# Kernel optimization log

Measured on AMD Instinct MI355X. Metric: run time of the kernel, lower is better.

Reference implementation:

```python
import math
import jax, jax.numpy as jnp
import numpy as np

T = 2048       # sequence_length
H = 2048       # hidden_size
NH = 32        # num_attention_heads
NKV = 8        # num_key_value_heads
HD = 64        # head_dim
SW = 128       # sliding_window
QM = NH // NKV # q_mult (GQA group size)
ROPE_THETA = 10000.0
EPS = 1e-5


def setup_inputs() -> dict:
    key = jax.random.key(0)
    k_x, k_s, k_qkv, k_out = jax.random.split(key, 4)
    x = jax.random.normal(k_x, (T, H), dtype=jnp.float32)
    scale = jnp.ones((H,), dtype=jnp.float32)
    sinks = jax.random.normal(k_s, (NH,), dtype=jnp.float32) * 0.02
    qkv_dim = HD * (NH + 2 * NKV)  # 3072
    qkv_kernel = jax.random.normal(k_qkv, (H, qkv_dim), dtype=jnp.float32) * (1.0 / math.sqrt(H))
    qkv_bias = jnp.zeros((qkv_dim,), dtype=jnp.float32)
    out_kernel = jax.random.normal(k_out, (H, H), dtype=jnp.float32) * (1.0 / math.sqrt(H))
    out_bias = jnp.zeros((H,), dtype=jnp.float32)
    # RoPE tables: [T, HD//2]
    half = HD // 2
    inv_freq = 1.0 / (ROPE_THETA ** (np.arange(half, dtype=np.float64) / half))
    ang = np.outer(np.arange(T, dtype=np.float64), inv_freq)
    cos_table = jnp.asarray(np.cos(ang), dtype=jnp.float32)
    sin_table = jnp.asarray(np.sin(ang), dtype=jnp.float32)
    # causal + sliding-window additive mask [T, T]
    qp = np.arange(T, dtype=np.int32)[:, None]
    kp = np.arange(T, dtype=np.int32)[None, :]
    m = np.where(kp > qp, -np.inf, 0.0) + np.where(qp - kp > SW, -np.inf, 0.0)
    mask = jnp.asarray(m, dtype=jnp.float32)
    return dict(x=x, scale=scale, sinks=sinks, qkv_kernel=qkv_kernel,
                qkv_bias=qkv_bias, out_kernel=out_kernel, out_bias=out_bias,
                cos_table=cos_table, sin_table=sin_table, mask=mask)


def _rmsnorm(x, scale):
    t = x.astype(jnp.float32)
    rms = jnp.sqrt(jnp.mean(t * t, axis=-1, keepdims=True) + EPS)
    return ((t / rms) * scale).astype(x.dtype)


def _rope(x, cos, sin):
    # x: [T, ..., HD]; split-half rotation as in the reference RotaryEmbedding
    shp = x.shape
    xr = x.reshape(shp[0], -1, HD)
    c = cos[:, None, :].astype(xr.dtype)
    s = sin[:, None, :].astype(xr.dtype)
    x1, x2 = jnp.split(xr, 2, axis=-1)
    y = jnp.concatenate([x1 * c - x2 * s, x2 * c + x1 * s], axis=-1)
    return y.reshape(shp)


def reference(x, scale, sinks, qkv_kernel, qkv_bias, out_kernel, out_bias,
              cos_table, sin_table, mask):
    normed = _rmsnorm(x, scale)
    qkv = normed @ qkv_kernel + qkv_bias                 # [T, 3072]
    q_end = NH * HD
    k_end = q_end + NKV * HD
    q = qkv[:, :q_end].reshape(T, NKV, QM, HD)           # [T, nkv, qm, hd]
    k = qkv[:, q_end:k_end].reshape(T, NKV, HD)          # [T, nkv, hd]
    v = qkv[:, k_end:].reshape(T, NKV, HD)               # [T, nkv, hd]
    q = _rope(q, cos_table, sin_table)
    k = _rope(k, cos_table, sin_table)
    sm_scale = 1.0 / math.sqrt(float(HD))
    # GQA attention without materializing repeated K/V
    logits = jnp.einsum('qnmd,knd->nmqk', q, k) * sm_scale  # [nkv, qm, T, T]
    logits = logits + mask[None, None, :, :]
    sink_col = jnp.broadcast_to(sinks.reshape(NKV, QM, 1, 1), (NKV, QM, T, 1))
    logits = jnp.concatenate([logits, sink_col], axis=-1)   # [nkv, qm, T, T+1]
    weights = jax.nn.softmax(logits, axis=-1)[..., :-1]     # drop sink column
    attn = jnp.einsum('nmqk,knd->qnmd', weights, v).reshape(T, NH * HD)
    projected = attn @ out_kernel + out_bias
    return x + projected
```

## Files before the change

### kernel.cpp

```cpp
#include <hip/hip_runtime.h>
#include <hip/hip_bf16.h>
#include <stdint.h>

typedef __bf16 bf16_t;
typedef __attribute__((ext_vector_type(8))) __bf16 bf16x8;
typedef __attribute__((ext_vector_type(4))) __bf16 bf16x4;
typedef __attribute__((ext_vector_type(4))) float f32x4;

static constexpr int T_SEQ = 2048;
static constexpr int HID   = 2048;
static constexpr int NHEAD = 32;
static constexpr int NKVH  = 8;
static constexpr int HDIM  = 64;
static constexpr int QKVD  = 3072;

__device__ inline f32x4 mfma16(bf16x8 a, bf16x8 b, f32x4 c) {
    return __builtin_amdgcn_mfma_f32_16x16x32_bf16(a, b, c, 0, 0, 0);
}

__device__ inline void load_lds16(const bf16_t* g, bf16_t* l) {
    __builtin_amdgcn_global_load_lds(
        (const __attribute__((address_space(1))) void*)g,
        (__attribute__((address_space(3))) void*)l, 16, 0, 0);
}

__global__ __launch_bounds__(256) void prep_kernel(const float* __restrict__ Wq,
                                                   const float* __restrict__ Wo,
                                                   bf16_t* __restrict__ Tq,
                                                   bf16_t* __restrict__ To,
                                                   const float* __restrict__ x,
                                                   const float* __restrict__ scale,
                                                   bf16_t* __restrict__ normed) {
    __shared__ float tile[64 * 65];
    int b = blockIdx.x;
    const int t = threadIdx.x;
    if (b < 2560) {
        const float* in; bf16_t* outw; int NN, KK, bx, by;
        if (b < 1536) { in = Wq; outw = Tq; NN = QKVD; KK = HID; bx = b % 48; by = b / 48; }
        else { b -= 1536; in = Wo; outw = To; NN = HID; KK = HID; bx = b % 32; by = b / 32; }
        const int c4 = (t & 15) * 4;
#pragma unroll
        for (int i = 0; i < 4; ++i) {
            int r = (t >> 4) + i * 16;
            float4 v = *(const float4*)(in + (size_t)(by*64 + r) * NN + bx*64 + c4);
            tile[r*65 + c4 + 0] = v.x; tile[r*65 + c4 + 1] = v.y;
            tile[r*65 + c4 + 2] = v.z; tile[r*65 + c4 + 3] = v.w;
        }
        __syncthreads();
        const int kc = t & 7;
#pragma unroll
        for (int i = 0; i < 2; ++i) {
            int n = (t >> 3) + i * 32;
            bf16x8 o;
#pragma unroll
            for (int j = 0; j < 8; ++j) o[j] = (bf16_t)tile[(kc*8 + j)*65 + n];
            *(bf16x8*)(outw + (size_t)(bx*64 + n) * KK + by*64 + kc*8) = o;
        }
    } else {
        int row = b - 2560;
        const float4* x4 = (const float4*)(x + (size_t)row * HID);
        const float4* s4 = (const float4*)scale;
        float4 v0 = x4[t], v1 = x4[t + 256];
        float ss = v0.x*v0.x + v0.y*v0.y + v0.z*v0.z + v0.w*v0.w
                 + v1.x*v1.x + v1.y*v1.y + v1.z*v1.z + v1.w*v1.w;
#pragma unroll
        for (int off = 32; off > 0; off >>= 1) ss += __shfl_down(ss, off);
        if ((t & 63) == 0) tile[t >> 6] = ss;
        __syncthreads();
        float total = tile[0] + tile[1] + tile[2] + tile[3];
        float inv = rsqrtf(total * (1.0f / HID) + 1e-5f);
        float4 sc0 = s4[t], sc1 = s4[t + 256];
        bf16_t* outr = normed + (size_t)row * HID;
        bf16x4 o0, o1;
        o0.x = (bf16_t)(v0.x*inv*sc0.x); o0.y = (bf16_t)(v0.y*inv*sc0.y);
        o0.z = (bf16_t)(v0.z*inv*sc0.z); o0.w = (bf16_t)(v0.w*inv*sc0.w);
        o1.x = (bf16_t)(v1.x*inv*sc1.x); o1.y = (bf16_t)(v1.y*inv*sc1.y);
        o1.z = (bf16_t)(v1.z*inv*sc1.z); o1.w = (bf16_t)(v1.w*inv*sc1.w);
        *(bf16x4*)(outr + 4*t)        = o0;
        *(bf16x4*)(outr + 1024 + 4*t) = o1;
    }
}

__global__ __launch_bounds__(256) void gemm_splitk(const bf16_t* __restrict__ A,
                                                   const bf16_t* __restrict__ Bt,
                                                   bf16_t* __restrict__ Cpart,
                                                   int M, int N, int K) {
    __shared__ __align__(16) bf16_t Asm[2 * 128 * 32];
    __shared__ __align__(16) bf16_t Bsm[2 * 128 * 32];
    const int tid = threadIdx.x;
    const int bm = blockIdx.y * 128, bn = blockIdx.x * 128;
    const int kh = K >> 1;
    const int kb = blockIdx.z * kh;
    const int lane = tid & 63, wave = tid >> 6;
    const int wm = (wave & 1) * 64, wn = (wave >> 1) * 64;
    const int lm = lane & 15, quad = lane >> 4;

    f32x4 acc[4][4];
#pragma unroll
    for (int i = 0; i < 4; ++i)
#pragma unroll
        for (int j = 0; j < 4; ++j) acc[i][j] = (f32x4){0.f, 0.f, 0.f, 0.f};

    const int cid0 = tid, cid1 = tid + 256;
    const int r0 = cid0 >> 2, c0 = (cid0 & 3) ^ ((r0 >> 1) & 3);
    const int r1 = cid1 >> 2, c1 = (cid1 & 3) ^ ((r1 >> 1) & 3);
    const bf16_t* Ab = A  + (size_t)bm * K + kb;
    const bf16_t* Bb = Bt + (size_t)bn * K + kb;
    const size_t ga0 = (size_t)r0 * K + c0 * 8;
    const size_t ga1 = (size_t)r1 * K + c1 * 8;
    bf16_t* ldsA0a = &Asm[wave * 512];
    bf16_t* ldsA0b = &Asm[2048 + wave * 512];
    bf16_t* ldsA1a = &Asm[4096 + wave * 512];
    bf16_t* ldsA1b = &Asm[4096 + 2048 + wave * 512];
    bf16_t* ldsB0a = &Bsm[wave * 512];
    bf16_t* ldsB0b = &Bsm[2048 + wave * 512];
    bf16_t* ldsB1a = &Bsm[4096 + wave * 512];
    bf16_t* ldsB1b = &Bsm[4096 + 2048 + wave * 512];
    const int swz = (quad ^ ((lm >> 1) & 3)) * 8;

    for (int k0 = 0; k0 < kh; k0 += 64) {
        load_lds16(Ab + ga0 + k0,      ldsA0a);
        load_lds16(Ab + ga1 + k0,      ldsA0b);
        load_lds16(Ab + ga0 + k0 + 32, ldsA1a);
        load_lds16(Ab + ga1 + k0 + 32, ldsA1b);
        load_lds16(Bb + ga0 + k0,      ldsB0a);
        load_lds16(Bb + ga1 + k0,      ldsB0b);
        load_lds16(Bb + ga0 + k0 + 32, ldsB1a);
        load_lds16(Bb + ga1 + k0 + 32, ldsB1b);
        __syncthreads();
#pragma unroll
        for (int ks = 0; ks < 2; ++ks) {
            bf16x8 af[4], bfr[4];
#pragma unroll
            for (int i = 0; i < 4; ++i)
                af[i]  = *(const bf16x8*)&Asm[ks*4096 + (wm + i*16 + lm)*32 + swz];
#pragma unroll
            for (int j = 0; j < 4; ++j)
                bfr[j] = *(const bf16x8*)&Bsm[ks*4096 + (wn + j*16 + lm)*32 + swz];
#pragma unroll
            for (int i = 0; i < 4; ++i)
#pragma unroll
                for (int j = 0; j < 4; ++j) acc[i][j] = mfma16(af[i], bfr[j], acc[i][j]);
        }
        __syncthreads();
    }

    bf16_t* Cp = Cpart + (size_t)blockIdx.z * M * N;
#pragma unroll
    for (int i = 0; i < 4; ++i) {
        int gr = bm + wm + i*16 + quad*4;
#pragma unroll
        for (int j = 0; j < 4; ++j) {
            int gc = bn + wn + j*16 + lm;
#pragma unroll
            for (int r = 0; r < 4; ++r)
                Cp[(size_t)(gr + r)*N + gc] = (bf16_t)acc[i][j][r];
        }
    }
}

__global__ __launch_bounds__(192) void rope_split(const bf16_t* __restrict__ qp0,
                                                  const bf16_t* __restrict__ qp1,
                                                  const float* __restrict__ qbias,
                                                  const float* __restrict__ cost,
                                                  const float* __restrict__ sint,
                                                  bf16_t* __restrict__ Qb,
                                                  bf16_t* __restrict__ Kb,
                                                  bf16_t* __restrict__ Vb) {
    const int t = blockIdx.x;
    const int hr = threadIdx.x >> 2, p0 = (threadIdx.x & 3) * 8;
    const bf16_t* r0 = qp0 + (size_t)t * QKVD + hr * 64;
    const bf16_t* r1 = qp1 + (size_t)t * QKVD + hr * 64;
    bf16x8 a1 = *(const bf16x8*)(r0 + p0);
    bf16x8 a2 = *(const bf16x8*)(r0 + p0 + 32);
    bf16x8 b1 = *(const bf16x8*)(r1 + p0);
    bf16x8 b2 = *(const bf16x8*)(r1 + p0 + 32);
    const float* qb = qbias + hr * 64;
    float x1[8], x2[8];
#pragma unroll
    for (int j = 0; j < 8; ++j) {
        x1[j] = (float)a1[j] + (float)b1[j] + qb[p0 + j];
        x2[j] = (float)a2[j] + (float)b2[j] + qb[p0 + j + 32];
    }
    bf16x8 w1, w2;
    if (hr < 40) {
        const float* c = cost + (size_t)t * 32 + p0;
        const float* s = sint + (size_t)t * 32 + p0;
#pragma unroll
        for (int j = 0; j < 8; ++j) {
            float cc = c[j], ss = s[j];
            w1[j] = (bf16_t)(x1[j]*cc - x2[j]*ss);
            w2[j] = (bf16_t)(x2[j]*cc + x1[j]*ss);
        }
    } else {
#pragma unroll
        for (int j = 0; j < 8; ++j) { w1[j] = (bf16_t)x1[j]; w2[j] = (bf16_t)x2[j]; }
    }
    bf16_t* dst;
    if (hr < 32)      dst = Qb + ((size_t)t*NHEAD + hr)      * HDIM;
    else if (hr < 40) dst = Kb + ((size_t)t*NKVH + (hr-32))  * HDIM;
    else              dst = Vb + ((size_t)t*NKVH + (hr-40))  * HDIM;
    *(bf16x8*)(dst + p0)      = w1;
    *(bf16x8*)(dst + p0 + 32) = w2;
}

__global__ __launch_bounds__(256) void combine_out(const bf16_t* __restrict__ p0,
                                                   const bf16_t* __restrict__ p1,
                                                   const float* __restrict__ bias,
                                                   const float* __restrict__ x,
                                                   float* __restrict__ out) {
    const int n4 = T_SEQ * HID / 4;
    for (int i4 = blockIdx.x * 256 + threadIdx.x; i4 < n4; i4 += gridDim.x * 256) {
        bf16x4 a = *(const bf16x4*)(p0 + (size_t)i4 * 4);
        bf16x4 b = *(const bf16x4*)(p1 + (size_t)i4 * 4);
        float4 xv = *(const float4*)(x + (size_t)i4 * 4);
        int col4 = (i4 * 4) & (HID - 1);
        float4 bi = *(const float4*)(bias + col4);
        float4 o;
        o.x = (float)a.x + (float)b.x + bi.x + xv.x;
        o.y = (float)a.y + (float)b.y + bi.y + xv.y;
        o.z = (float)a.z + (float)b.z + bi.z + xv.z;
        o.w = (float)a.w + (float)b.w + bi.w + xv.w;
        *(float4*)(out + (size_t)i4 * 4) = o;
    }
}

__global__ __launch_bounds__(256) void attn_kernel(const bf16_t* __restrict__ Qb,
                                                   const bf16_t* __restrict__ Kb,
                                                   const bf16_t* __restrict__ Vb,
                                                   const float* __restrict__ sinks,
                                                   bf16_t* __restrict__ attnb) {
    __shared__ __align__(16) bf16_t Vt[64 * 200];
    __shared__ __align__(16) bf16_t Ws[64 * 200];

    const int tid = threadIdx.x;
    const int qt = blockIdx.x, h = blockIdx.y;
    const int qs = qt * 64;
    const int nkv = h >> 2;

    {
        const int off = (tid >> 5) * 8;
#pragma unroll
        for (int it = 0; it < 3; ++it) {
            int j2 = (tid & 31) + 32 * it;
            int kg0 = qs - 128 + 2*j2;     if (kg0 < 0) kg0 = 0;
            int kg1 = qs - 128 + 2*j2 + 1; if (kg1 < 0) kg1 = 0;
            union { uint4 u; bf16_t e[8]; } v0, v1;
            v0.u = *(const uint4*)(Vb + ((size_t)kg0*NKVH + nkv)*HDIM + off);
            v1.u = *(const uint4*)(Vb + ((size_t)kg1*NKVH + nkv)*HDIM + off);
#pragma unroll
            for (int r = 0; r < 8; ++r) {
                union { uint u; bf16_t e[2]; } p;
                p.e[0] = v0.e[r]; p.e[1] = v1.e[r];
                *(uint*)&Vt[(off + r)*200 + 2*j2] = p.u;
            }
        }
    }

    const int lane = tid & 63, wave = tid >> 6;
    const int lm = lane & 15, quad = lane >> 4;
    const int w16 = wave * 16;

    f32x4 S[12];
#pragma unroll
    for (int jt = 0; jt < 12; ++jt) S[jt] = (f32x4){0.f, 0.f, 0.f, 0.f};
    const bf16_t* Qrow = Qb + ((size_t)(qs + w16 + lm)*NHEAD + h)*HDIM + quad*8;
    int krow[12];
#pragma unroll
    for (int jt = 0; jt < 12; ++jt) {
        int kg = qs - 128 + jt*16 + lm;
        krow[jt] = kg < 0 ? 0 : kg;
    }
#pragma unroll
    for (int ks = 0; ks < 2; ++ks) {
        bf16x8 aq = *(const bf16x8*)(Qrow + ks*32);
#pragma unroll
        for (int jt = 0; jt < 12; ++jt) {
            bf16x8 bk = *(const bf16x8*)(Kb + ((size_t)krow[jt]*NKVH + nkv)*HDIM + ks*32 + quad*8);
            S[jt] = mfma16(aq, bk, S[jt]);
        }
    }

    const float sink = sinks[h];
#pragma unroll
    for (int reg = 0; reg < 4; ++reg) {
        const int qg = qs + w16 + quad*4 + reg;
        float mx = -1e30f;
#pragma unroll
        for (int jt = 0; jt < 12; ++jt) {
            int kg = qs - 128 + jt*16 + lm;
            float sv = S[jt][reg] * 0.125f;
            bool valid = (kg >= 0) && (kg <= qg) && (qg - kg <= 128);
            sv = valid ? sv : -1e30f;
            S[jt][reg] = sv;
            mx = fmaxf(mx, sv);
        }
#pragma unroll
        for (int off = 1; off < 16; off <<= 1) mx = fmaxf(mx, __shfl_xor(mx, off));
        float M = fmaxf(mx, sink);
        float sum = 0.f;
#pragma unroll
        for (int jt = 0; jt < 12; ++jt) {
            float e = __expf(S[jt][reg] - M);
            S[jt][reg] = e; sum += e;
        }
#pragma unroll
        for (int off = 1; off < 16; off <<= 1) sum += __shfl_xor(sum, off);
        float rden = 1.f / (sum + __expf(sink - M));
#pragma unroll
        for (int jt = 0; jt < 12; ++jt)
            Ws[(w16 + quad*4 + reg)*200 + jt*16 + lm] = (bf16_t)(S[jt][reg] * rden);
    }
    __syncthreads();

    f32x4 O[4];
#pragma unroll
    for (int nt = 0; nt < 4; ++nt) O[nt] = (f32x4){0.f, 0.f, 0.f, 0.f};
#pragma unroll
    for (int ks = 0; ks < 6; ++ks) {
        bf16x8 aw = *(const bf16x8*)&Ws[(w16 + lm)*200 + ks*32 + quad*8];
#pragma unroll
        for (int nt = 0; nt < 4; ++nt) {
            bf16x8 bv = *(const bf16x8*)&Vt[(nt*16 + lm)*200 + ks*32 + quad*8];
            O[nt] = mfma16(aw, bv, O[nt]);
        }
    }
#pragma unroll
    for (int nt = 0; nt < 4; ++nt)
#pragma unroll
        for (int reg = 0; reg < 4; ++reg)
            attnb[(size_t)(qs + w16 + quad*4 + reg)*HID + h*HDIM + nt*16 + lm] =
                (bf16_t)(O[nt][reg]);
}

extern "C" void kernel_launch(void* const* d_in, const int* in_sizes, int n_in,
                              void* d_out, int out_size, void* d_ws, size_t ws_size,
                              hipStream_t stream) {
    (void)in_sizes; (void)n_in; (void)out_size; (void)ws_size;
    const float* x          = (const float*)d_in[0];
    const float* scale      = (const float*)d_in[1];
    const float* sinks      = (const float*)d_in[2];
    const float* qkv_kernel = (const float*)d_in[3];
    const float* qkv_bias   = (const float*)d_in[4];
    const float* out_kernel = (const float*)d_in[5];
    const float* out_bias   = (const float*)d_in[6];
    const float* cos_t      = (const float*)d_in[7];
    const float* sin_t      = (const float*)d_in[8];
    float* out = (float*)d_out;

    char* ws = (char*)d_ws;
    const size_t MiB = 1048576;
    bf16_t* Wt_out = (bf16_t*)(ws);
    bf16_t* Wt_qkv = (bf16_t*)(ws + 8*MiB);
    bf16_t* attnb  = (bf16_t*)(ws + 8*MiB);
    bf16_t* normed = (bf16_t*)(ws + 20*MiB);
    bf16_t* qkvp   = (bf16_t*)(ws + 28*MiB);
    bf16_t* outp   = (bf16_t*)(ws + 28*MiB);
    bf16_t* Qb     = (bf16_t*)(ws + 52*MiB);
    bf16_t* Kb     = (bf16_t*)(ws + 60*MiB);
    bf16_t* Vb     = (bf16_t*)(ws + 62*MiB);

    prep_kernel<<<4608, 256, 0, stream>>>(qkv_kernel, out_kernel, Wt_qkv, Wt_out,
                                          x, scale, normed);
    gemm_splitk<<<dim3(QKVD/128, T_SEQ/128, 2), 256, 0, stream>>>(normed, Wt_qkv, qkvp,
                                                                  T_SEQ, QKVD, HID);
    rope_split<<<T_SEQ, 192, 0, stream>>>(qkvp, qkvp + (size_t)T_SEQ*QKVD, qkv_bias,
                                          cos_t, sin_t, Qb, Kb, Vb);
    attn_kernel<<<dim3(T_SEQ/64, NHEAD), 256, 0, stream>>>(Qb, Kb, Vb, sinks, attnb);
    gemm_splitk<<<dim3(HID/128, T_SEQ/128, 2), 256, 0, stream>>>(attnb, Wt_out, outp,
                                                                 T_SEQ, HID, HID);
    combine_out<<<2048, 256, 0, stream>>>(outp, outp + (size_t)T_SEQ*HID, out_bias, x, out);
}
```

Measured before the change: 221.4 us.

## Pipeline split-K GEMM with triple-buffered LDS and async prefetch

New measurement: 224.6 us. No clear change (+1.4%).

```diff
diff --git a/kernel.cpp b/kernel.cpp
--- a/kernel.cpp
+++ b/kernel.cpp
@@ -85,8 +85,8 @@
                                                    const bf16_t* __restrict__ Bt,
                                                    bf16_t* __restrict__ Cpart,
                                                    int M, int N, int K) {
-    __shared__ __align__(16) bf16_t Asm[2 * 128 * 32];
-    __shared__ __align__(16) bf16_t Bsm[2 * 128 * 32];
+    __shared__ __align__(16) bf16_t Asm[3 * 128 * 32];
+    __shared__ __align__(16) bf16_t Bsm[3 * 128 * 32];
     const int tid = threadIdx.x;
     const int bm = blockIdx.y * 128, bn = blockIdx.x * 128;
     const int kh = K >> 1;
@@ -108,42 +108,49 @@
     const bf16_t* Bb = Bt + (size_t)bn * K + kb;
     const size_t ga0 = (size_t)r0 * K + c0 * 8;
     const size_t ga1 = (size_t)r1 * K + c1 * 8;
-    bf16_t* ldsA0a = &Asm[wave * 512];
-    bf16_t* ldsA0b = &Asm[2048 + wave * 512];
-    bf16_t* ldsA1a = &Asm[4096 + wave * 512];
-    bf16_t* ldsA1b = &Asm[4096 + 2048 + wave * 512];
-    bf16_t* ldsB0a = &Bsm[wave * 512];
-    bf16_t* ldsB0b = &Bsm[2048 + wave * 512];
-    bf16_t* ldsB1a = &Bsm[4096 + wave * 512];
-    bf16_t* ldsB1b = &Bsm[4096 + 2048 + wave * 512];
     const int swz = (quad ^ ((lm >> 1) & 3)) * 8;
-
-    for (int k0 = 0; k0 < kh; k0 += 64) {
-        load_lds16(Ab + ga0 + k0,      ldsA0a);
-        load_lds16(Ab + ga1 + k0,      ldsA0b);
-        load_lds16(Ab + ga0 + k0 + 32, ldsA1a);
-        load_lds16(Ab + ga1 + k0 + 32, ldsA1b);
-        load_lds16(Bb + ga0 + k0,      ldsB0a);
-        load_lds16(Bb + ga1 + k0,      ldsB0b);
-        load_lds16(Bb + ga0 + k0 + 32, ldsB1a);
-        load_lds16(Bb + ga1 + k0 + 32, ldsB1b);
-        __syncthreads();
-#pragma unroll
-        for (int ks = 0; ks < 2; ++ks) {
-            bf16x8 af[4], bfr[4];
-#pragma unroll
-            for (int i = 0; i < 4; ++i)
-                af[i]  = *(const bf16x8*)&Asm[ks*4096 + (wm + i*16 + lm)*32 + swz];
-#pragma unroll
-            for (int j = 0; j < 4; ++j)
-                bfr[j] = *(const bf16x8*)&Bsm[ks*4096 + (wn + j*16 + lm)*32 + swz];
-#pragma unroll
-            for (int i = 0; i < 4; ++i)
-#pragma unroll
-                for (int j = 0; j < 4; ++j) acc[i][j] = mfma16(af[i], bfr[j], acc[i][j]);
-        }
-        __syncthreads();
-    }
+    const int ldso = wave * 512;
+
+    const int nsteps = kh >> 5;
+
+#define STAGE(buf, k0) do {                               \
+        bf16_t* la_ = &Asm[(buf) * 4096];                 \
+        bf16_t* lb_ = &Bsm[(buf) * 4096];                 \
+        load_lds16(Ab + ga0 + (k0), la_ + ldso);          \
+        load_lds16(Ab + ga1 + (k0), la_ + 2048 + ldso);   \
+        load_lds16(Bb + ga0 + (k0), lb_ + ldso);          \
+        load_lds16(Bb + ga1 + (k0), lb_ + 2048 + ldso);   \
+    } while (0)
+
+    STAGE(0, 0);
+    STAGE(1, 32);
+
+    int cur = 0, nxt = 2;
+    for (int t = 0; t < nsteps; ++t) {
+        if (t + 1 < nsteps) asm volatile("s_waitcnt vmcnt(4)" ::: "memory");
+        else                asm volatile("s_waitcnt vmcnt(0)" ::: "memory");
+        __builtin_amdgcn_s_barrier();
+        __builtin_amdgcn_sched_barrier(0);
+        if (t + 2 < nsteps) STAGE(nxt, (t + 2) * 32);
+
+        const bf16_t* __restrict__ Abase = &Asm[cur * 4096];
+        const bf16_t* __restrict__ Bbase = &Bsm[cur * 4096];
+        bf16x8 af[4], bfr[4];
+#pragma unroll
+        for (int i = 0; i < 4; ++i)
+            af[i]  = *(const bf16x8*)&Abase[(wm + i*16 + lm)*32 + swz];
+#pragma unroll
+        for (int j = 0; j < 4; ++j)
+            bfr[j] = *(const bf16x8*)&Bbase[(wn + j*16 + lm)*32 + swz];
+#pragma unroll
+        for (int i = 0; i < 4; ++i)
+#pragma unroll
+            for (int j = 0; j < 4; ++j) acc[i][j] = mfma16(af[i], bfr[j], acc[i][j]);
+
+        cur = (cur == 2) ? 0 : cur + 1;
+        nxt = (nxt == 2) ? 0 : nxt + 1;
+    }
+#undef STAGE
 
     bf16_t* Cp = Cpart + (size_t)blockIdx.z * M * N;
 #pragma unroll
```

## Fuse QKV projection with bias and RoPE epilogue, drop split-K and rope kernel

Applied to the files above, without the earlier changes.

Result: no change. 220.2 us (-0.6%).

```diff
diff --git a/kernel.cpp b/kernel.cpp
--- a/kernel.cpp
+++ b/kernel.cpp
@@ -78,6 +78,109 @@
         o1.z = (bf16_t)(v1.z*inv*sc1.z); o1.w = (bf16_t)(v1.w*inv*sc1.w);
         *(bf16x4*)(outr + 4*t)        = o0;
         *(bf16x4*)(outr + 1024 + 4*t) = o1;
+    }
+}
+
+__global__ __launch_bounds__(256) void gemm_qkv_rope(const bf16_t* __restrict__ A,
+                                                     const bf16_t* __restrict__ Bt,
+                                                     const float* __restrict__ qkvb,
+                                                     const float* __restrict__ cost,
+                                                     const float* __restrict__ sint,
+                                                     bf16_t* __restrict__ Qb,
+                                                     bf16_t* __restrict__ Kb,
+                                                     bf16_t* __restrict__ Vb) {
+    __shared__ __align__(16) bf16_t Asm[2 * 128 * 32];
+    __shared__ __align__(16) bf16_t Bsm[2 * 128 * 32];
+    const int K = HID;
+    const int tid = threadIdx.x;
+    const int bm = blockIdx.y * 128, bn = blockIdx.x * 128;
+    const int lane = tid & 63, wave = tid >> 6;
+    const int wm = (wave & 1) * 64, wn = (wave >> 1) * 64;
+    const int lm = lane & 15, quad = lane >> 4;
+
+    f32x4 acc[4][4];
+#pragma unroll
+    for (int i = 0; i < 4; ++i)
+#pragma unroll
+        for (int j = 0; j < 4; ++j) acc[i][j] = (f32x4){0.f, 0.f, 0.f, 0.f};
+
+    const int cid0 = tid, cid1 = tid + 256;
+    const int r0 = cid0 >> 2, c0 = (cid0 & 3) ^ ((r0 >> 1) & 3);
+    const int r1 = cid1 >> 2, c1 = (cid1 & 3) ^ ((r1 >> 1) & 3);
+    const bf16_t* Ab = A  + (size_t)bm * K;
+    const bf16_t* Bb = Bt + (size_t)bn * K;
+    const size_t ga0 = (size_t)r0 * K + c0 * 8;
+    const size_t ga1 = (size_t)r1 * K + c1 * 8;
+    bf16_t* ldsA0a = &Asm[wave * 512];
+    bf16_t* ldsA0b = &Asm[2048 + wave * 512];
+    bf16_t* ldsA1a = &Asm[4096 + wave * 512];
+    bf16_t* ldsA1b = &Asm[4096 + 2048 + wave * 512];
+    bf16_t* ldsB0a = &Bsm[wave * 512];
+    bf16_t* ldsB0b = &Bsm[2048 + wave * 512];
+    bf16_t* ldsB1a = &Bsm[4096 + wave * 512];
+    bf16_t* ldsB1b = &Bsm[4096 + 2048 + wave * 512];
+    const int swz = (quad ^ ((lm >> 1) & 3)) * 8;
+
+    for (int k0 = 0; k0 < K; k0 += 64) {
+        load_lds16(Ab + ga0 + k0,      ldsA0a);
+        load_lds16(Ab + ga1 + k0,      ldsA0b);
+        load_lds16(Ab + ga0 + k0 + 32, ldsA1a);
+        load_lds16(Ab + ga1 + k0 + 32, ldsA1b);
+        load_lds16(Bb + ga0 + k0,      ldsB0a);
+        load_lds16(Bb + ga1 + k0,      ldsB0b);
+        load_lds16(Bb + ga0 + k0 + 32, ldsB1a);
+        load_lds16(Bb + ga1 + k0 + 32, ldsB1b);
+        __syncthreads();
+#pragma unroll
+        for (int ks = 0; ks < 2; ++ks) {
+            bf16x8 af[4], bfr[4];
+#pragma unroll
+            for (int i = 0; i < 4; ++i)
+                af[i]  = *(const bf16x8*)&Asm[ks*4096 + (wm + i*16 + lm)*32 + swz];
+#pragma unroll
+            for (int j = 0; j < 4; ++j)
+                bfr[j] = *(const bf16x8*)&Bsm[ks*4096 + (wn + j*16 + lm)*32 + swz];
+#pragma unroll
+            for (int i = 0; i < 4; ++i)
+#pragma unroll
+                for (int j = 0; j < 4; ++j) acc[i][j] = mfma16(af[i], bfr[j], acc[i][j]);
+        }
+        __syncthreads();
+    }
+
+    const int gcb = bn + wn;
+    bf16_t* dstbase; int cstride, coff; bool dorope;
+    if (bn < 2048)      { dstbase = Qb; cstride = 2048; coff = 0;    dorope = true;  }
+    else if (bn < 2560) { dstbase = Kb; cstride = 512;  coff = 2048; dorope = true;  }
+    else                { dstbase = Vb; cstride = 512;  coff = 2560; dorope = false; }
+    float bj[4];
+#pragma unroll
+    for (int j = 0; j < 4; ++j) bj[j] = qkvb[gcb + j*16 + lm];
+    const int colb = gcb - coff + lm;
+
+#pragma unroll
+    for (int i = 0; i < 4; ++i) {
+        const int tr = bm + wm + i*16 + quad*4;
+#pragma unroll
+        for (int r = 0; r < 4; ++r) {
+            const int t = tr + r;
+            bf16_t* drow = dstbase + (size_t)t * cstride + colb;
+            if (dorope) {
+                float c0 = cost[t*32 + lm],      s0 = sint[t*32 + lm];
+                float c1 = cost[t*32 + 16 + lm], s1 = sint[t*32 + 16 + lm];
+                float x10 = acc[i][0][r] + bj[0], x20 = acc[i][2][r] + bj[2];
+                float x11 = acc[i][1][r] + bj[1], x21 = acc[i][3][r] + bj[3];
+                drow[0]  = (bf16_t)(x10*c0 - x20*s0);
+                drow[16] = (bf16_t)(x11*c1 - x21*s1);
+                drow[32] = (bf16_t)(x20*c0 + x10*s0);
+                drow[48] = (bf16_t)(x21*c1 + x11*s1);
+            } else {
+                drow[0]  = (bf16_t)(acc[i][0][r] + bj[0]);
+                drow[16] = (bf16_t)(acc[i][1][r] + bj[1]);
+                drow[32] = (bf16_t)(acc[i][2][r] + bj[2]);
+                drow[48] = (bf16_t)(acc[i][3][r] + bj[3]);
+            }
+        }
     }
 }
 
@@ -157,51 +260,6 @@
                 Cp[(size_t)(gr + r)*N + gc] = (bf16_t)acc[i][j][r];
         }
     }
-}
-
-__global__ __launch_bounds__(192) void rope_split(const bf16_t* __restrict__ qp0,
-                                                  const bf16_t* __restrict__ qp1,
-                                                  const float* __restrict__ qbias,
-                                                  const float* __restrict__ cost,
-                                                  const float* __restrict__ sint,
-                                                  bf16_t* __restrict__ Qb,
-                                                  bf16_t* __restrict__ Kb,
-                                                  bf16_t* __restrict__ Vb) {
-    const int t = blockIdx.x;
-    const int hr = threadIdx.x >> 2, p0 = (threadIdx.x & 3) * 8;
-    const bf16_t* r0 = qp0 + (size_t)t * QKVD + hr * 64;
-    const bf16_t* r1 = qp1 + (size_t)t * QKVD + hr * 64;
-    bf16x8 a1 = *(const bf16x8*)(r0 + p0);
-    bf16x8 a2 = *(const bf16x8*)(r0 + p0 + 32);
-    bf16x8 b1 = *(const bf16x8*)(r1 + p0);
-    bf16x8 b2 = *(const bf16x8*)(r1 + p0 + 32);
-    const float* qb = qbias + hr * 64;
-    float x1[8], x2[8];
-#pragma unroll
-    for (int j = 0; j < 8; ++j) {
-        x1[j] = (float)a1[j] + (float)b1[j] + qb[p0 + j];
-        x2[j] = (float)a2[j] + (float)b2[j] + qb[p0 + j + 32];
-    }
-    bf16x8 w1, w2;
-    if (hr < 40) {
-        const float* c = cost + (size_t)t * 32 + p0;
-        const float* s = sint + (size_t)t * 32 + p0;
-#pragma unroll
-        for (int j = 0; j < 8; ++j) {
-            float cc = c[j], ss = s[j];
-            w1[j] = (bf16_t)(x1[j]*cc - x2[j]*ss);
-            w2[j] = (bf16_t)(x2[j]*cc + x1[j]*ss);
-        }
-    } else {
-#pragma unroll
-        for (int j = 0; j < 8; ++j) { w1[j] = (bf16_t)x1[j]; w2[j] = (bf16_t)x2[j]; }
-    }
-    bf16_t* dst;
-    if (hr < 32)      dst = Qb + ((size_t)t*NHEAD + hr)      * HDIM;
-    else if (hr < 40) dst = Kb + ((size_t)t*NKVH + (hr-32))  * HDIM;
-    else              dst = Vb + ((size_t)t*NKVH + (hr-40))  * HDIM;
-    *(bf16x8*)(dst + p0)      = w1;
-    *(bf16x8*)(dst + p0 + 32) = w2;
 }
 
 __global__ __launch_bounds__(256) void combine_out(const bf16_t* __restrict__ p0,
@@ -271,6 +329,7 @@
         int kg = qs - 128 + jt*16 + lm;
         krow[jt] = kg < 0 ? 0 : kg;
     }
+    __builtin_amdgcn_s_setprio(1);
 #pragma unroll
     for (int ks = 0; ks < 2; ++ks) {
         bf16x8 aq = *(const bf16x8*)(Qrow + ks*32);
@@ -280,6 +339,7 @@
             S[jt] = mfma16(aq, bk, S[jt]);
         }
     }
+    __builtin_amdgcn_s_setprio(0);
 
     const float sink = sinks[h];
 #pragma unroll
@@ -316,6 +376,7 @@
     f32x4 O[4];
 #pragma unroll
     for (int nt = 0; nt < 4; ++nt) O[nt] = (f32x4){0.f, 0.f, 0.f, 0.f};
+    __builtin_amdgcn_s_setprio(1);
 #pragma unroll
     for (int ks = 0; ks < 6; ++ks) {
         bf16x8 aw = *(const bf16x8*)&Ws[(w16 + lm)*200 + ks*32 + quad*8];
@@ -325,6 +386,7 @@
             O[nt] = mfma16(aw, bv, O[nt]);
         }
     }
+    __builtin_amdgcn_s_setprio(0);
 #pragma unroll
     for (int nt = 0; nt < 4; ++nt)
 #pragma unroll
@@ -354,18 +416,16 @@
     bf16_t* Wt_qkv = (bf16_t*)(ws + 8*MiB);
     bf16_t* attnb  = (bf16_t*)(ws + 8*MiB);
     bf16_t* normed = (bf16_t*)(ws + 20*MiB);
-    bf16_t* qkvp   = (bf16_t*)(ws + 28*MiB);
-    bf16_t* outp   = (bf16_t*)(ws + 28*MiB);
-    bf16_t* Qb     = (bf16_t*)(ws + 52*MiB);
-    bf16_t* Kb     = (bf16_t*)(ws + 60*MiB);
-    bf16_t* Vb     = (bf16_t*)(ws + 62*MiB);
+    bf16_t* Qb     = (bf16_t*)(ws + 28*MiB);
+    bf16_t* Kb     = (bf16_t*)(ws + 36*MiB);
+    bf16_t* Vb     = (bf16_t*)(ws + 38*MiB);
+    bf16_t* outp   = (bf16_t*)(ws + 40*MiB);
 
     prep_kernel<<<4608, 256, 0, stream>>>(qkv_kernel, out_kernel, Wt_qkv, Wt_out,
                                           x, scale, normed);
-    gemm_splitk<<<dim3(QKVD/128, T_SEQ/128, 2), 256, 0, stream>>>(normed, Wt_qkv, qkvp,
-                                                                  T_SEQ, QKVD, HID);
-    rope_split<<<T_SEQ, 192, 0, stream>>>(qkvp, qkvp + (size_t)T_SEQ*QKVD, qkv_bias,
-                                          cos_t, sin_t, Qb, Kb, Vb);
+    gemm_qkv_rope<<<dim3(QKVD/128, T_SEQ/128), 256, 0, stream>>>(normed, Wt_qkv,
+                                                                 qkv_bias, cos_t, sin_t,
+                                                                 Qb, Kb, Vb);
     attn_kernel<<<dim3(T_SEQ/64, NHEAD), 256, 0, stream>>>(Qb, Kb, Vb, sinks, attnb);
     gemm_splitk<<<dim3(HID/128, T_SEQ/128, 2), 256, 0, stream>>>(attnb, Wt_out, outp,
                                                                  T_SEQ, HID, HID);
```
